# Performance work log

Measured on AMD Instinct MI355X. Metric: run time of the kernel, lower is better.

## Reference

```python
import jax, jax.numpy as jnp
import numpy as np

D_MODEL = 192
NODE_NUM = 64
DEPTH = 2
ALPHA = 0.05
NUM_LAYERS = 2
LN_EPS = 1e-5


def _gcn(x, p):
    # x: [N, in_dim*D_MODEL]; faithful port of GCN.forward (eval mode)
    nv1, nv2, ws, bs, wm, bm, we, be, wl, bl, g, b = p
    N = x.shape[0]
    in_dim = x.shape[1] // D_MODEL
    adp = jax.nn.softmax(jax.nn.relu(nv1 @ nv2), axis=1)            # [V,V]
    adj = adp + jnp.eye(NODE_NUM, dtype=x.dtype)
    a = adj / adj.sum(1, keepdims=True)                              # row-normalized
    h0 = jax.lax.conv_general_dilated(
        x.reshape(N, in_dim, D_MODEL), ws, (1,), 'VALID',
        dimension_numbers=('NCH', 'OIH', 'NCH')) + bs[None, :, None]  # [N,C,V]
    h = h0
    outs = [h0]
    for _ in range(DEPTH):
        h = ALPHA * h0 + (1.0 - ALPHA) * jnp.einsum('ncw,vw->ncv', h, a)
        outs.append(h)
    ho = jnp.concatenate(outs, axis=1)                               # [N,(DEPTH+1)C,V]
    ho = jax.nn.gelu(jnp.einsum('ncv,oc->nov', ho, wm) + bm[None, :, None], approximate=False)
    ho = jnp.einsum('ncv,oc->nov', ho, we) + be[None, :, None]       # [N,6,V]
    ho = jnp.einsum('nov,dv->nod', ho, wl) + bl                      # [N,6,D]
    mu = ho.mean(-1, keepdims=True)
    var = ((ho - mu) ** 2).mean(-1, keepdims=True)                   # biased, like torch LN
    ho = (ho - mu) / jnp.sqrt(var + LN_EPS) * g + b
    return ho.reshape(N, 6 * D_MODEL)


def _encoder(inp4, flag, layer_params):
    x = jnp.transpose(inp4, (2, 0, 1, 3)) if flag == 1 else jnp.transpose(inp4, (1, 0, 2, 3))
    W, B, O, D = x.shape
    L = W + O - 1
    N = W * B
    # input_transfer: shift row r by r along the slice axis
    place = jax.vmap(lambda xr, r: jax.lax.dynamic_update_slice(
        jnp.zeros((B, L, D), x.dtype), xr, (0, r, 0)))
    a = place(x, jnp.arange(W)).reshape(N, L, D)
    layer0_output = None
    output_all = None
    rows_layers, cols_layers = [], []
    for layer in range(NUM_LAYERS):
        if layer >= 1:
            a = output_all  # eval mode: F.dropout is identity
            if layer == 1:
                layer0_output = a
        p = layer_params[layer]

        def step(carry, x_t, p=p):
            h_row, h_col = carry
            gate = _gcn(jnp.concatenate([h_row, h_col, x_t], axis=-1), p)  # [N,6D]
            sg = jax.nn.sigmoid(gate[:, :4 * D])
            tg = jnp.tanh(gate[:, 4 * D:])
            ug_r, og_r, ug_c, og_c = jnp.split(sg, 4, axis=-1)
            ig_r, ig_c = jnp.split(tg, 2, axis=-1)
            h_row = jnp.tanh((1.0 - ug_r) * h_row + ug_r * ig_r) * og_r
            h_col = jnp.tanh((1.0 - ug_c) * h_col + ug_c * ig_c) * og_c
            out_s = jnp.concatenate([h_row, h_col], axis=-1)
            # col hidden is saved pre-roll, rolled for next step
            return (h_row, jnp.roll(h_col, B, axis=0)), (out_s, h_row, h_col)

        init = (jnp.zeros((N, D), x.dtype), jnp.zeros((N, D), x.dtype))
        _, (outs, hrows, hcols) = jax.lax.scan(step, init, jnp.swapaxes(a, 0, 1))
        output_all = jnp.swapaxes(outs, 0, 1)                        # [N,L,2D]
        if layer >= 1:
            output_all = output_all + layer0_output
        # rows saved at slice s>=O-1 from block loc = s-O+1
        rows = hrows.reshape(L, W, B, D)[jnp.arange(O - 1, L), jnp.arange(W)]  # [W,B,D]
        # cols saved at slice s>=W-1 from last batch block
        cols = hcols[W - 1:, (W - 1) * B:, :]                        # [O,B,D]
        rows_layers.append(rows)
        cols_layers.append(cols)
    hidden_row_all = jnp.stack(rows_layers).transpose(2, 0, 1, 3)    # [B,layers,W,D]
    hidden_col_all = jnp.stack(cols_layers).transpose(2, 0, 1, 3)    # [B,layers,O,D]
    if flag == 1:
        return output_all, hidden_col_all, hidden_row_all
    return output_all, hidden_row_all, hidden_col_all


def setup_inputs() -> dict:
    key = jax.random.key(0)
    ks = jax.random.split(key, 20)
    idx = [0]
    def nxt():
        k = ks[idx[0]]
        idx[0] += 1
        return k
    B, W, O = 8, 24, 48
    K = D_MODEL - NODE_NUM + 1  # 129
    cc, sc, nd = 16, 32, 40
    d = {"input": jax.random.normal(nxt(), (B, W, O, D_MODEL), dtype=jnp.float32)}
    for li, in_dim in enumerate([3, 4]):
        d[f"nodevec1_{li}"] = jax.random.normal(nxt(), (NODE_NUM, nd), dtype=jnp.float32)
        d[f"nodevec2_{li}"] = jax.random.normal(nxt(), (nd, NODE_NUM), dtype=jnp.float32)
        d[f"w_start_{li}"] = jax.random.normal(nxt(), (cc, in_dim, K), dtype=jnp.float32) * 0.05
        d[f"b_start_{li}"] = jnp.zeros((cc,), jnp.float32)
        d[f"w_mlp_{li}"] = jax.random.normal(nxt(), (sc, (DEPTH + 1) * cc), dtype=jnp.float32) * 0.05
        d[f"b_mlp_{li}"] = jnp.zeros((sc,), jnp.float32)
        d[f"w_end_{li}"] = jax.random.normal(nxt(), (6, sc), dtype=jnp.float32) * 0.05
        d[f"b_end_{li}"] = jnp.zeros((6,), jnp.float32)
        d[f"w_lin_{li}"] = jax.random.normal(nxt(), (D_MODEL, NODE_NUM), dtype=jnp.float32) * 0.05
        d[f"b_lin_{li}"] = jnp.zeros((D_MODEL,), jnp.float32)
        d[f"gamma_{li}"] = jnp.ones((D_MODEL,), jnp.float32)
        d[f"beta_{li}"] = jnp.zeros((D_MODEL,), jnp.float32)
    d["flag"] = 0
    return d


def reference(input, nodevec1_0, nodevec2_0, w_start_0, b_start_0, w_mlp_0, b_mlp_0,
              w_end_0, b_end_0, w_lin_0, b_lin_0, gamma_0, beta_0,
              nodevec1_1, nodevec2_1, w_start_1, b_start_1, w_mlp_1, b_mlp_1,
              w_end_1, b_end_1, w_lin_1, b_lin_1, gamma_1, beta_1, flag):
    p0 = (nodevec1_0, nodevec2_0, w_start_0, b_start_0, w_mlp_0, b_mlp_0,
          w_end_0, b_end_0, w_lin_0, b_lin_0, gamma_0, beta_0)
    p1 = (nodevec1_1, nodevec2_1, w_start_1, b_start_1, w_mlp_1, b_mlp_1,
          w_end_1, b_end_1, w_lin_1, b_lin_1, gamma_1, beta_1)
    return _encoder(input, flag, (p0, p1))
```

## Files before the change

### kernel.cpp

```cpp
#include <hip/hip_runtime.h>
#include <hip/hip_bf16.h>

#define NT 512
typedef unsigned short u16;
typedef unsigned long long u64;

__device__ __forceinline__ u16 tobf(float x) {
  union { __hip_bfloat16 h; u16 u; } cv;
  cv.h = __float2bfloat16(x);
  return cv.u;
}
__device__ __forceinline__ float frombf(u16 u) {
  return __uint_as_float(((unsigned)u) << 16);
}
__device__ __forceinline__ float sigf(float x) {
  return __builtin_amdgcn_rcpf(1.f + __builtin_amdgcn_exp2f(-1.4426950408889634f * x));
}
__device__ __forceinline__ float tanh_fast(float x) {
  return 1.f - 2.f * __builtin_amdgcn_rcpf(1.f + __builtin_amdgcn_exp2f(2.8853900817779268f * x));
}
__device__ __forceinline__ void lds_fence() {
  asm volatile("s_waitcnt lgkmcnt(0)" ::: "memory");
  __builtin_amdgcn_sched_barrier(0);
}
__device__ __forceinline__ void bar_light() {
  asm volatile("s_waitcnt lgkmcnt(0)" ::: "memory");
  __builtin_amdgcn_s_barrier();
  asm volatile("" ::: "memory");
}

__device__ __forceinline__ void conv4(const float* __restrict__ wrow,
                                      const float* __restrict__ xin,
                                      float& a0, float& a1, float& a2, float& a3) {
  float4 xc = *(const float4*)xin;
  for (int k4 = 0; k4 < 128; k4 += 4) {
    float4 wv = *(const float4*)(wrow + k4);
    float4 xn = *(const float4*)(xin + k4 + 4);
    a0 = fmaf(wv.w, xc.w, fmaf(wv.z, xc.z, fmaf(wv.y, xc.y, fmaf(wv.x, xc.x, a0))));
    a1 = fmaf(wv.w, xn.x, fmaf(wv.z, xc.w, fmaf(wv.y, xc.z, fmaf(wv.x, xc.y, a1))));
    a2 = fmaf(wv.w, xn.y, fmaf(wv.z, xn.x, fmaf(wv.y, xc.w, fmaf(wv.x, xc.z, a2))));
    a3 = fmaf(wv.w, xn.z, fmaf(wv.z, xn.y, fmaf(wv.y, xn.x, fmaf(wv.x, xc.w, a3))));
    xc = xn;
  }
  float wk = wrow[128];
  a0 = fmaf(wk, xc.x, a0); a1 = fmaf(wk, xc.y, a1);
  a2 = fmaf(wk, xc.z, a2); a3 = fmaf(wk, xc.w, a3);
}

struct SeqArgs {
  const float* input;
  const float* nv1_0; const float* nv2_0; const float* nv1_1; const float* nv2_1;
  const float* w_start0; const float* b_start0; const float* w_mlp0; const float* b_mlp0;
  const float* w_end0;   const float* b_end0;   const float* w_lin0; const float* b_lin0;
  const float* gamma0;   const float* beta0;
  const float* w_start1; const float* b_start1; const float* w_mlp1; const float* b_mlp1;
  const float* w_end1;   const float* b_end1;   const float* w_lin1; const float* b_lin1;
  const float* gamma1;   const float* beta1;
  u64*   HCOL2;
  int*   prog;
  float* out_all; float* out_hrow; float* out_hcol;
};

__global__ __launch_bounds__(NT, 2) void seq_kernel(SeqArgs A) {
  const int n = blockIdx.x, w = n >> 3, b = n & 7, tid = threadIdx.x;
  const int pred = (n + 184) % 192;
  const int succ = (n + 8) % 192;

  __shared__ __align__(16) float sCIN[384];
  __shared__ __align__(16) float sXB[2][384];
  __shared__ __align__(16) float sWSf[64 * 132];
  __shared__ __align__(16) float sAT[4096];
  __shared__ __align__(16) float sH[2][1024];
  __shared__ __align__(16) float sPreP[2048];
  __shared__ __align__(16) float sAbuf[4928];
  float* const sPart = sAbuf;
  float* const sG    = sAbuf;
  float* const sH2c  = sAbuf + 2048;
  float* const sE    = sAbuf + 2048;
  float* const sY    = sAbuf;
  float* const smWE  = sAbuf + 3072;
  float* const smBE  = sAbuf + 3264;
  float* const smWM  = sAbuf + 3328;

  for (int layer = 0; layer < 2; ++layer) {
    const int in_dim = 3 + layer;
    const int P = in_dim - 1;
    const float* nv1    = layer ? A.nv1_1    : A.nv1_0;
    const float* nv2    = layer ? A.nv2_1    : A.nv2_0;
    const float* wstart = layer ? A.w_start1 : A.w_start0;
    const float* bs     = layer ? A.b_start1 : A.b_start0;
    const float* wm     = layer ? A.w_mlp1   : A.w_mlp0;
    const float* bm     = layer ? A.b_mlp1   : A.b_mlp0;
    const float* we     = layer ? A.w_end1   : A.w_end0;
    const float* be     = layer ? A.b_end1   : A.b_end0;
    const float* wl     = layer ? A.w_lin1   : A.w_lin0;
    const float* bl     = layer ? A.b_lin1   : A.b_lin0;
    const float* gm     = layer ? A.gamma1   : A.gamma0;
    const float* bt     = layer ? A.beta1    : A.beta0;

    for (int idx = tid; idx < 4096; idx += NT) {
      int v = idx >> 6, ww = idx & 63;
      float s = 0.f;
      for (int j = 0; j < 40; ++j) s = fmaf(nv1[v*40 + j], nv2[j*64 + ww], s);
      sAbuf[idx] = fmaxf(s, 0.f);
    }
    __syncthreads();
    if (tid < 64) {
      const int v = tid;
      float m = -1e30f;
      for (int ww = 0; ww < 64; ++ww) m = fmaxf(m, sAbuf[v*64 + ww]);
      float s = 0.f;
      for (int ww = 0; ww < 64; ++ww) { float e = expf(sAbuf[v*64 + ww] - m); sAbuf[v*64 + ww] = e; s += e; }
      float inv = 1.f / s, rs = 1.f;
      for (int ww = 0; ww < 64; ++ww) rs += sAbuf[v*64 + ww] * inv;
      float irs = 1.f / rs;
      for (int ww = 0; ww < 64; ++ww) {
        float a = sAbuf[v*64 + ww] * inv + ((ww == v) ? 1.f : 0.f);
        sAT[ww*64 + v] = a * irs;
      }
    }
    __syncthreads();
    for (int idx = tid; idx < 16*in_dim*132; idx += NT) {
      int row = idx / 132, k = idx - row*132;
      sWSf[idx] = (k < 129) ? frombf(tobf(wstart[((row & 15)*in_dim + (row >> 4))*129 + k])) : 0.f;
    }
    for (int idx = tid; idx < 1536; idx += NT) { int o = idx/48, c = idx - o*48; smWM[o*50 + c] = wm[idx]; }
    for (int idx = tid; idx < 192; idx += NT) smWE[idx] = we[idx];
    if (tid < 6) smBE[tid] = be[tid];
    for (int d = tid; d < 384; d += NT) sCIN[d] = 0.f;

    const int v_p = tid & 63;
    const int o0  = tid >> 6;
    const float bmv0 = bm[o0], bmv1 = bm[o0 + 8], bmv2 = bm[o0 + 16], bmv3 = bm[o0 + 24];
    float blv = 0.f, gmv = 1.f, btv = 0.f;
    if (tid < 384) blv = bl[(tid >= 192) ? tid - 192 : tid];
    if (tid < 192) { gmv = gm[tid]; btv = bt[tid]; }
    float bs_r[2];
    bs_r[0] = bs[tid >> 6];
    bs_r[1] = bs[(tid >> 6) + 8];
    __syncthreads();

    {
      if (layer == 0) {
        int o = 0 - w;
        for (int d = tid; d < 192; d += NT)
          sXB[0][d] = (o >= 0 && o < 48) ? A.input[(((size_t)(b*24 + w)*48 + o)*192) + d] : 0.f;
      } else {
        for (int d = tid; d < 384; d += NT)
          sXB[0][d] = A.out_all[((size_t)n*71 + 0)*384 + d];
      }
      bar_light();
      const int nslots = P << 8;
      for (int s = tid; s < nslots; s += NT) {
        const int cidx = s >> 4;
        const int p = cidx >> 4, c = cidx & 15;
        const int vg = s & 15;
        const int ich = (p == 0) ? 0 : (p + 1);
        const float* xin = ((p == 0) ? &sCIN[0] : &sXB[0][(p-1)*192]) + vg*4;
        float a0 = 0.f, a1 = 0.f, a2 = 0.f, a3 = 0.f;
        conv4(&sWSf[(ich*16 + c)*132], xin, a0, a1, a2, a3);
        float* dst = (p == 0) ? &sPart[c*64 + vg*4] : &sPreP[(p-1)*1024 + c*64 + vg*4];
        *(float4*)dst = make_float4(a0, a1, a2, a3);
      }
      bar_light();
      {
        const int c0 = tid >> 6, v = tid & 63;
        float sum0 = bs_r[0], sum1 = bs_r[1];
        sum0 += sPart[c0*64 + v];
        sum1 += sPart[(c0+8)*64 + v];
        for (int p = 1; p < P; ++p) {
          sum0 += sPreP[(p-1)*1024 + c0*64 + v];
          sum1 += sPreP[(p-1)*1024 + (c0+8)*64 + v];
        }
        sH[0][ c0     *64 + v] = sum0;
        sH[0][(c0 + 8)*64 + v] = sum1;
      }
      bar_light();
    }

    for (int t = 0; t < 71; ++t) {
      const int S = layer*71 + t;

      float xpa = 0.f, xpb = 0.f;
      if (t < 70 && tid >= 256 && tid < 448) {
        const int d = tid - 256;
        if (layer == 0) {
          int o = (t + 1) - w;
          if (o >= 0 && o < 48)
            xpa = A.input[(((size_t)(b*24 + w)*48 + o)*192) + d];
        } else {
          const float* xr = A.out_all + ((size_t)n*71 + (t+1))*384;
          xpa = xr[d];
          xpb = xr[192 + d];
        }
      }
      if (t > 0) {
        if (tid < 192) {
          const u64* src = &A.HCOL2[((size_t)((S-1) & 15)*192 + pred)*192 + tid];
          u64 v = __hip_atomic_load(src, __ATOMIC_RELAXED, __HIP_MEMORY_SCOPE_AGENT);
          while ((unsigned)(v >> 32) != (unsigned)S) {
            __builtin_amdgcn_s_sleep(1);
            v = __hip_atomic_load(src, __ATOMIC_RELAXED, __HIP_MEMORY_SCOPE_AGENT);
          }
          __builtin_amdgcn_sched_barrier(0);
          asm volatile("" ::: "memory");
          sCIN[192 + tid] = __uint_as_float((unsigned)v);
        } else if (tid == 448 && S >= 16) {
          while (__hip_atomic_load(&A.prog[succ*32], __ATOMIC_RELAXED, __HIP_MEMORY_SCOPE_AGENT) < S - 15)
            __builtin_amdgcn_s_sleep(2);
        }
        bar_light();
        if (tid == 0)
          __hip_atomic_store(&A.prog[n*32], S, __ATOMIC_RELAXED, __HIP_MEMORY_SCOPE_AGENT);
      } else if (S >= 16) {
        if (tid == 448) {
          while (__hip_atomic_load(&A.prog[succ*32], __ATOMIC_RELAXED, __HIP_MEMORY_SCOPE_AGENT) < S - 15)
            __builtin_amdgcn_s_sleep(2);
        }
      }

      {
        const int c = tid >> 5, vg2 = tid & 31;
        const int vbase = c*64 + vg2*2;
        const float* xin = &sCIN[192 + vg2*2];
        const float* wrow = &sWSf[(16 + c)*132];
        float a0 = sH[0][vbase], a1 = sH[0][vbase + 1];
        float2 xc = *(const float2*)xin;
        for (int k2 = 0; k2 < 128; k2 += 2) {
          float2 wv = *(const float2*)(wrow + k2);
          float2 xn = *(const float2*)(xin + k2 + 2);
          a0 = fmaf(wv.y, xc.y, fmaf(wv.x, xc.x, a0));
          a1 = fmaf(wv.y, xn.x, fmaf(wv.x, xc.y, a1));
          xc = xn;
        }
        float wk = wrow[128];
        a0 = fmaf(wk, xc.x, a0); a1 = fmaf(wk, xc.y, a1);
        sH[0][vbase] = a0; sH[0][vbase + 1] = a1;
      }
      lds_fence();
      {
        const int c0 = o0 * 2;
        float pa0 = 0.f, pa1 = 0.f;
        for (int w4 = 0; w4 < 64; w4 += 4) {
          float a0v = sAT[(w4+0)*64 + v_p];
          float a1v = sAT[(w4+1)*64 + v_p];
          float a2v = sAT[(w4+2)*64 + v_p];
          float a3v = sAT[(w4+3)*64 + v_p];
          float4 h0v = *(const float4*)&sH[0][ c0      *64 + w4];
          float4 h1v = *(const float4*)&sH[0][(c0 + 1 )*64 + w4];
          pa0 = fmaf(h0v.x, a0v, pa0); pa0 = fmaf(h0v.y, a1v, pa0);
          pa0 = fmaf(h0v.z, a2v, pa0); pa0 = fmaf(h0v.w, a3v, pa0);
          pa1 = fmaf(h1v.x, a0v, pa1); pa1 = fmaf(h1v.y, a1v, pa1);
          pa1 = fmaf(h1v.z, a2v, pa1); pa1 = fmaf(h1v.w, a3v, pa1);
        }
        float h0a = sH[0][ c0      *64 + v_p];
        float h0b = sH[0][(c0 + 1 )*64 + v_p];
        sH[1][ c0      *64 + v_p] = fmaf(0.95f, pa0, 0.05f * h0a);
        sH[1][(c0 + 1 )*64 + v_p] = fmaf(0.95f, pa1, 0.05f * h0b);
        lds_fence();
        float pb0 = 0.f, pb1 = 0.f;
        for (int w4 = 0; w4 < 64; w4 += 4) {
          float a0v = sAT[(w4+0)*64 + v_p];
          float a1v = sAT[(w4+1)*64 + v_p];
          float a2v = sAT[(w4+2)*64 + v_p];
          float a3v = sAT[(w4+3)*64 + v_p];
          float4 h0v = *(const float4*)&sH[1][ c0      *64 + w4];
          float4 h1v = *(const float4*)&sH[1][(c0 + 1 )*64 + w4];
          pb0 = fmaf(h0v.x, a0v, pb0); pb0 = fmaf(h0v.y, a1v, pb0);
          pb0 = fmaf(h0v.z, a2v, pb0); pb0 = fmaf(h0v.w, a3v, pb0);
          pb1 = fmaf(h1v.x, a0v, pb1); pb1 = fmaf(h1v.y, a1v, pb1);
          pb1 = fmaf(h1v.z, a2v, pb1); pb1 = fmaf(h1v.w, a3v, pb1);
        }
        sH2c[ c0      *64 + v_p] = fmaf(0.95f, pb0, 0.05f * h0a);
        sH2c[(c0 + 1 )*64 + v_p] = fmaf(0.95f, pb1, 0.05f * h0b);
      }
      bar_light();

      {
        float g0 = bmv0, g1 = bmv1, g2 = bmv2, g3 = bmv3;
#pragma unroll
        for (int c = 0; c < 16; ++c) {
          float h0v = sH[0][c*64 + v_p];
          float h1v = sH[1][c*64 + v_p];
          float h2v = sH2c[c*64 + v_p];
          g0 = fmaf(smWM[(o0     )*50 + c], h0v, fmaf(smWM[(o0     )*50 + 16 + c], h1v, fmaf(smWM[(o0     )*50 + 32 + c], h2v, g0)));
          g1 = fmaf(smWM[(o0 +  8)*50 + c], h0v, fmaf(smWM[(o0 +  8)*50 + 16 + c], h1v, fmaf(smWM[(o0 +  8)*50 + 32 + c], h2v, g1)));
          g2 = fmaf(smWM[(o0 + 16)*50 + c], h0v, fmaf(smWM[(o0 + 16)*50 + 16 + c], h1v, fmaf(smWM[(o0 + 16)*50 + 32 + c], h2v, g2)));
          g3 = fmaf(smWM[(o0 + 24)*50 + c], h0v, fmaf(smWM[(o0 + 24)*50 + 16 + c], h1v, fmaf(smWM[(o0 + 24)*50 + 32 + c], h2v, g3)));
        }
        g0 = 0.5f * g0 * (1.f + erff(g0 * 0.70710678118654752f));
        g1 = 0.5f * g1 * (1.f + erff(g1 * 0.70710678118654752f));
        g2 = 0.5f * g2 * (1.f + erff(g2 * 0.70710678118654752f));
        g3 = 0.5f * g3 * (1.f + erff(g3 * 0.70710678118654752f));
        sG[(o0     )*64 + v_p] = g0;
        sG[(o0 +  8)*64 + v_p] = g1;
        sG[(o0 + 16)*64 + v_p] = g2;
        sG[(o0 + 24)*64 + v_p] = g3;
      }
      bar_light();

      for (int idx = tid; idx < 384; idx += NT) {
        int o2 = idx >> 6, v = idx & 63;
        float acc = smBE[o2];
        for (int c = 0; c < 32; ++c) acc = fmaf(smWE[o2*32 + c], sG[c*64 + v], acc);
        sE[idx] = acc;
      }
      bar_light();

      if (tid < 384) {
        const int d  = (tid >= 192) ? tid - 192 : tid;
        const int r0 = (tid >= 192) ? 3 : 0;
        const float4* wrow = (const float4*)(wl + d*64);
        float y0 = blv, y1 = blv, y2 = blv;
        for (int q = 0; q < 16; ++q) {
          float4 wv = wrow[q];
          float4 e0 = *(const float4*)&sE[(r0+0)*64 + q*4];
          float4 e1 = *(const float4*)&sE[(r0+1)*64 + q*4];
          float4 e2 = *(const float4*)&sE[(r0+2)*64 + q*4];
          y0 = fmaf(e0.x,wv.x, fmaf(e0.y,wv.y, fmaf(e0.z,wv.z, fmaf(e0.w,wv.w, y0))));
          y1 = fmaf(e1.x,wv.x, fmaf(e1.y,wv.y, fmaf(e1.z,wv.z, fmaf(e1.w,wv.w, y1))));
          y2 = fmaf(e2.x,wv.x, fmaf(e2.y,wv.y, fmaf(e2.z,wv.z, fmaf(e2.w,wv.w, y2))));
        }
        sY[(r0+0)*192 + d] = y0;
        sY[(r0+1)*192 + d] = y1;
        sY[(r0+2)*192 + d] = y2;
      }
      bar_light();

      if (tid < 192) {
        const int r = tid >> 5, l32 = tid & 31;
        float sm = 0.f, sq = 0.f;
#pragma unroll
        for (int m = 0; m < 6; ++m) {
          float v = sY[r*192 + l32 + 32*m];
          sm += v; sq = fmaf(v, v, sq);
        }
#pragma unroll
        for (int off = 16; off >= 1; off >>= 1) {
          sm += __shfl_xor(sm, off);
          sq += __shfl_xor(sq, off);
        }
        if (l32 == 0) {
          float mu = sm * (1.f/192.f);
          float var = sq * (1.f/192.f) - mu*mu;
          sH[1][r] = mu;
          sH[1][8 + r] = rsqrtf(fmaxf(var, 0.f) + 1e-5f);
        }
      }
      bar_light();

      float hcn = 0.f;
      if (tid < 192) {
        const int d = tid;
        float y2 = fmaf((sY[2*192+d] - sH[1][2]) * sH[1][10], gmv, btv);
        float y3 = fmaf((sY[3*192+d] - sH[1][3]) * sH[1][11], gmv, btv);
        float y5 = fmaf((sY[5*192+d] - sH[1][5]) * sH[1][13], gmv, btv);
        float ugc = sigf(y2), ogc = sigf(y3), igc = tanh_fast(y5);
        float hc = sCIN[192 + d];
        hcn = tanh_fast(fmaf(ugc, igc, (1.f - ugc)*hc)) * ogc;
        u64 pk = ((u64)(unsigned)(S + 1) << 32) | (u64)__float_as_uint(hcn);
        __hip_atomic_store(&A.HCOL2[((size_t)(S & 15)*192 + n)*192 + d], pk,
                           __ATOMIC_RELAXED, __HIP_MEMORY_SCOPE_AGENT);
      } else if (t < 70 && tid >= 256 && tid < 448) {
        const int d = tid - 256;
        float* xbn = &sXB[(t+1) & 1][0];
        xbn[d] = xpa;
        if (layer == 1) xbn[192 + d] = xpb;
      }
      bar_light();

      if (tid < 192) {
        const int d = tid;
        float y0 = fmaf((sY[0*192+d] - sH[1][0]) * sH[1][8],  gmv, btv);
        float y1 = fmaf((sY[1*192+d] - sH[1][1]) * sH[1][9],  gmv, btv);
        float y4 = fmaf((sY[4*192+d] - sH[1][4]) * sH[1][12], gmv, btv);
        float ugr = sigf(y0), ogr = sigf(y1), igr = tanh_fast(y4);
        float hr = sCIN[d];
        float hrn = tanh_fast(fmaf(ugr, igr, (1.f - ugr)*hr)) * ogr;
        sCIN[d] = hrn;
        float* oa = A.out_all + ((size_t)n*71 + t)*384;
        if (layer == 0) { oa[d] = hrn; oa[192 + d] = hcn; }
        else {
          const float* xbt = &sXB[t & 1][0];
          oa[d] = hrn + xbt[d]; oa[192 + d] = hcn + xbt[192 + d];
        }
        if (t == 47 + w)
          A.out_hrow[(((size_t)b*2 + layer)*24 + w)*192 + d] = hrn;
        if (w == 23 && t >= 23)
          A.out_hcol[(((size_t)b*2 + layer)*48 + (t - 23))*192 + d] = hcn;
      } else if (t < 70 && tid >= 192 && tid < 448) {
        const int sl = tid - 192;
        const int nx = (P - 1) << 8;
        const float* xbn = &sXB[(t+1) & 1][0];
        for (int s = sl; s < nx; s += 256) {
          const int p = 1 + (s >> 8);
          const int c = (s >> 4) & 15, vg = s & 15;
          const int ich = p + 1;
          float a0 = 0.f, a1 = 0.f, a2 = 0.f, a3 = 0.f;
          conv4(&sWSf[(ich*16 + c)*132], &xbn[(p-1)*192 + vg*4], a0, a1, a2, a3);
          *(float4*)&sPreP[(p-1)*1024 + c*64 + vg*4] = make_float4(a0, a1, a2, a3);
        }
      }
      bar_light();

      if (t < 70) {
        if (tid < 256) {
          const int c = tid >> 4, vg = tid & 15;
          float a0 = 0.f, a1 = 0.f, a2 = 0.f, a3 = 0.f;
          conv4(&sWSf[c*132], &sCIN[vg*4], a0, a1, a2, a3);
          *(float4*)&sPart[c*64 + vg*4] = make_float4(a0, a1, a2, a3);
        }
        bar_light();
        {
          const int c0 = tid >> 6, v = tid & 63;
          float sum0 = bs_r[0], sum1 = bs_r[1];
          sum0 += sPart[c0*64 + v];
          sum1 += sPart[(c0+8)*64 + v];
          for (int p = 1; p < P; ++p) {
            sum0 += sPreP[(p-1)*1024 + c0*64 + v];
            sum1 += sPreP[(p-1)*1024 + (c0+8)*64 + v];
          }
          sH[0][ c0     *64 + v] = sum0;
          sH[0][(c0 + 8)*64 + v] = sum1;
        }
        bar_light();
      }
    }
    __syncthreads();
  }
}

extern "C" void kernel_launch(void* const* d_in, const int* in_sizes, int n_in,
                              void* d_out, int out_size, void* d_ws, size_t ws_size,
                              hipStream_t stream) {
  (void)in_sizes; (void)n_in; (void)out_size; (void)ws_size;
  char* ws = (char*)d_ws;
  int* prog  = (int*)ws;
  u64* HCOL2 = (u64*)(ws + 24576);

  (void)hipMemsetAsync(ws, 0, 24576 + 4718592, stream);

  SeqArgs A;
  A.input    = (const float*)d_in[0];
  A.nv1_0    = (const float*)d_in[1];  A.nv2_0 = (const float*)d_in[2];
  A.w_start0 = (const float*)d_in[3];  A.b_start0 = (const float*)d_in[4];
  A.w_mlp0   = (const float*)d_in[5];  A.b_mlp0   = (const float*)d_in[6];
  A.w_end0   = (const float*)d_in[7];  A.b_end0   = (const float*)d_in[8];
  A.w_lin0   = (const float*)d_in[9];  A.b_lin0   = (const float*)d_in[10];
  A.gamma0   = (const float*)d_in[11]; A.beta0    = (const float*)d_in[12];
  A.nv1_1    = (const float*)d_in[13]; A.nv2_1 = (const float*)d_in[14];
  A.w_start1 = (const float*)d_in[15]; A.b_start1 = (const float*)d_in[16];
  A.w_mlp1   = (const float*)d_in[17]; A.b_mlp1   = (const float*)d_in[18];
  A.w_end1   = (const float*)d_in[19]; A.b_end1   = (const float*)d_in[20];
  A.w_lin1   = (const float*)d_in[21]; A.b_lin1   = (const float*)d_in[22];
  A.gamma1   = (const float*)d_in[23]; A.beta1    = (const float*)d_in[24];
  A.HCOL2 = HCOL2; A.prog = prog;
  A.out_all  = (float*)d_out;
  A.out_hrow = (float*)d_out + 5234688;
  A.out_hcol = (float*)d_out + 5308416;

  seq_kernel<<<192, NT, 0, stream>>>(A);
}
```

Measured before the change: 2.672 ms.

## Restructure per-step schedule to cut barriers and overlap cross-block wait

```diff
diff --git a/kernel.cpp b/kernel.cpp
--- a/kernel.cpp
+++ b/kernel.cpp
@@ -67,7 +67,6 @@
   const int succ = (n + 8) % 192;
 
   __shared__ __align__(16) float sCIN[384];
-  __shared__ __align__(16) float sXB[2][384];
   __shared__ __align__(16) float sWSf[64 * 132];
   __shared__ __align__(16) float sAT[4096];
   __shared__ __align__(16) float sH[2][1024];
@@ -78,6 +77,7 @@
   float* const sH2c  = sAbuf + 2048;
   float* const sE    = sAbuf + 2048;
   float* const sY    = sAbuf;
+  float* const sLN   = sAbuf + 2432;
   float* const smWE  = sAbuf + 3072;
   float* const smBE  = sAbuf + 3264;
   float* const smWM  = sAbuf + 3328;
@@ -132,99 +132,55 @@
     const int v_p = tid & 63;
     const int o0  = tid >> 6;
     const float bmv0 = bm[o0], bmv1 = bm[o0 + 8], bmv2 = bm[o0 + 16], bmv3 = bm[o0 + 24];
+    const float bs_c = bs[tid >> 5];
     float blv = 0.f, gmv = 1.f, btv = 0.f;
     if (tid < 384) blv = bl[(tid >= 192) ? tid - 192 : tid];
     if (tid < 192) { gmv = gm[tid]; btv = bt[tid]; }
-    float bs_r[2];
-    bs_r[0] = bs[tid >> 6];
-    bs_r[1] = bs[(tid >> 6) + 8];
     __syncthreads();
 
-    {
-      if (layer == 0) {
-        int o = 0 - w;
-        for (int d = tid; d < 192; d += NT)
-          sXB[0][d] = (o >= 0 && o < 48) ? A.input[(((size_t)(b*24 + w)*48 + o)*192) + d] : 0.f;
-      } else {
-        for (int d = tid; d < 384; d += NT)
-          sXB[0][d] = A.out_all[((size_t)n*71 + 0)*384 + d];
-      }
-      bar_light();
-      const int nslots = P << 8;
-      for (int s = tid; s < nslots; s += NT) {
-        const int cidx = s >> 4;
-        const int p = cidx >> 4, c = cidx & 15;
-        const int vg = s & 15;
-        const int ich = (p == 0) ? 0 : (p + 1);
-        const float* xin = ((p == 0) ? &sCIN[0] : &sXB[0][(p-1)*192]) + vg*4;
+    if (tid >= 256) {
+      const int i = tid - 256;
+      *(float4*)&sPart[i*4] = make_float4(0.f, 0.f, 0.f, 0.f);
+    } else if (tid >= 192) {
+    }
+    if (tid >= 192 && tid < 448) {
+      const int sl = tid - 192;
+      const int nx = (P - 1) << 8;
+      for (int s = sl; s < nx; s += 256) {
+        const int p = 1 + (s >> 8), c = (s >> 4) & 15, vg = s & 15;
         float a0 = 0.f, a1 = 0.f, a2 = 0.f, a3 = 0.f;
-        conv4(&sWSf[(ich*16 + c)*132], xin, a0, a1, a2, a3);
-        float* dst = (p == 0) ? &sPart[c*64 + vg*4] : &sPreP[(p-1)*1024 + c*64 + vg*4];
-        *(float4*)dst = make_float4(a0, a1, a2, a3);
-      }
-      bar_light();
-      {
-        const int c0 = tid >> 6, v = tid & 63;
-        float sum0 = bs_r[0], sum1 = bs_r[1];
-        sum0 += sPart[c0*64 + v];
-        sum1 += sPart[(c0+8)*64 + v];
-        for (int p = 1; p < P; ++p) {
-          sum0 += sPreP[(p-1)*1024 + c0*64 + v];
-          sum1 += sPreP[(p-1)*1024 + (c0+8)*64 + v];
-        }
-        sH[0][ c0     *64 + v] = sum0;
-        sH[0][(c0 + 8)*64 + v] = sum1;
-      }
-      bar_light();
-    }
+        if (layer == 0) {
+          int o = 0 - w;
+          if (o >= 0 && o < 48)
+            conv4(&sWSf[((p+1)*16 + c)*132],
+                  A.input + (((size_t)(b*24 + w)*48 + o)*192) + vg*4, a0, a1, a2, a3);
+        } else {
+          conv4(&sWSf[((p+1)*16 + c)*132],
+                A.out_all + ((size_t)n*71 + 0)*384 + (p-1)*192 + vg*4, a0, a1, a2, a3);
+        }
+        *(float4*)&sPreP[(p-1)*1024 + c*64 + vg*4] = make_float4(a0, a1, a2, a3);
+      }
+    }
+    if (tid == 0 && layer == 1) {
+      while (__hip_atomic_load(&A.prog[succ*32], __ATOMIC_RELAXED, __HIP_MEMORY_SCOPE_AGENT) < 56)
+        __builtin_amdgcn_s_sleep(2);
+    }
+    bar_light();
 
     for (int t = 0; t < 71; ++t) {
       const int S = layer*71 + t;
-
-      float xpa = 0.f, xpb = 0.f;
-      if (t < 70 && tid >= 256 && tid < 448) {
-        const int d = tid - 256;
-        if (layer == 0) {
-          int o = (t + 1) - w;
-          if (o >= 0 && o < 48)
-            xpa = A.input[(((size_t)(b*24 + w)*48 + o)*192) + d];
-        } else {
-          const float* xr = A.out_all + ((size_t)n*71 + (t+1))*384;
-          xpa = xr[d];
-          xpb = xr[192 + d];
-        }
-      }
-      if (t > 0) {
-        if (tid < 192) {
-          const u64* src = &A.HCOL2[((size_t)((S-1) & 15)*192 + pred)*192 + tid];
-          u64 v = __hip_atomic_load(src, __ATOMIC_RELAXED, __HIP_MEMORY_SCOPE_AGENT);
-          while ((unsigned)(v >> 32) != (unsigned)S) {
-            __builtin_amdgcn_s_sleep(1);
-            v = __hip_atomic_load(src, __ATOMIC_RELAXED, __HIP_MEMORY_SCOPE_AGENT);
-          }
-          __builtin_amdgcn_sched_barrier(0);
-          asm volatile("" ::: "memory");
-          sCIN[192 + tid] = __uint_as_float((unsigned)v);
-        } else if (tid == 448 && S >= 16) {
-          while (__hip_atomic_load(&A.prog[succ*32], __ATOMIC_RELAXED, __HIP_MEMORY_SCOPE_AGENT) < S - 15)
-            __builtin_amdgcn_s_sleep(2);
-        }
-        bar_light();
-        if (tid == 0)
-          __hip_atomic_store(&A.prog[n*32], S, __ATOMIC_RELAXED, __HIP_MEMORY_SCOPE_AGENT);
-      } else if (S >= 16) {
-        if (tid == 448) {
-          while (__hip_atomic_load(&A.prog[succ*32], __ATOMIC_RELAXED, __HIP_MEMORY_SCOPE_AGENT) < S - 15)
-            __builtin_amdgcn_s_sleep(2);
-        }
-      }
 
       {
         const int c = tid >> 5, vg2 = tid & 31;
         const int vbase = c*64 + vg2*2;
+        float a0 = bs_c + sPart[vbase];
+        float a1 = bs_c + sPart[vbase + 1];
+        for (int p = 1; p < P; ++p) {
+          a0 += sPreP[(p-1)*1024 + vbase];
+          a1 += sPreP[(p-1)*1024 + vbase + 1];
+        }
         const float* xin = &sCIN[192 + vg2*2];
         const float* wrow = &sWSf[(16 + c)*132];
-        float a0 = sH[0][vbase], a1 = sH[0][vbase + 1];
         float2 xc = *(const float2*)xin;
         for (int k2 = 0; k2 < 128; k2 += 2) {
           float2 wv = *(const float2*)(wrow + k2);
@@ -299,17 +255,18 @@
       }
       bar_light();
 
-      for (int idx = tid; idx < 384; idx += NT) {
-        int o2 = idx >> 6, v = idx & 63;
+      if (tid < 384) {
+        int o2 = tid >> 6, v = tid & 63;
         float acc = smBE[o2];
         for (int c = 0; c < 32; ++c) acc = fmaf(smWE[o2*32 + c], sG[c*64 + v], acc);
-        sE[idx] = acc;
+        sE[tid] = acc;
       }
       bar_light();
 
       if (tid < 384) {
         const int d  = (tid >= 192) ? tid - 192 : tid;
         const int r0 = (tid >= 192) ? 3 : 0;
+        const int part = (tid >= 192) ? ((tid - 192) >> 6) : (tid >> 6);
         const float4* wrow = (const float4*)(wl + d*64);
         float y0 = blv, y1 = blv, y2 = blv;
         for (int q = 0; q < 16; ++q) {
@@ -324,106 +281,102 @@
         sY[(r0+0)*192 + d] = y0;
         sY[(r0+1)*192 + d] = y1;
         sY[(r0+2)*192 + d] = y2;
+        float ys0 = y0, ys1 = y1, ys2 = y2;
+        float q0 = y0*y0, q1 = y1*y1, q2 = y2*y2;
+#pragma unroll
+        for (int off = 32; off >= 1; off >>= 1) {
+          ys0 += __shfl_xor(ys0, off); q0 += __shfl_xor(q0, off);
+          ys1 += __shfl_xor(ys1, off); q1 += __shfl_xor(q1, off);
+          ys2 += __shfl_xor(ys2, off); q2 += __shfl_xor(q2, off);
+        }
+        if ((tid & 63) == 0) {
+          sLN[(r0+0)*6 + part] = ys0; sLN[(r0+0)*6 + 3 + part] = q0;
+          sLN[(r0+1)*6 + part] = ys1; sLN[(r0+1)*6 + 3 + part] = q1;
+          sLN[(r0+2)*6 + part] = ys2; sLN[(r0+2)*6 + 3 + part] = q2;
+        }
       }
       bar_light();
 
       if (tid < 192) {
-        const int r = tid >> 5, l32 = tid & 31;
-        float sm = 0.f, sq = 0.f;
+        const int d = tid;
+        float* oa = A.out_all + ((size_t)n*71 + t)*384;
+        float r0v = 0.f, r1v = 0.f;
+        if (layer == 1) { r0v = oa[d]; r1v = oa[192 + d]; }
+        float muA[6], sgA[6];
 #pragma unroll
-        for (int m = 0; m < 6; ++m) {
-          float v = sY[r*192 + l32 + 32*m];
-          sm += v; sq = fmaf(v, v, sq);
-        }
-#pragma unroll
-        for (int off = 16; off >= 1; off >>= 1) {
-          sm += __shfl_xor(sm, off);
-          sq += __shfl_xor(sq, off);
-        }
-        if (l32 == 0) {
+        for (int r = 0; r < 6; ++r) {
+          float sm = (sLN[r*6 + 0] + sLN[r*6 + 1]) + sLN[r*6 + 2];
+          float sq = (sLN[r*6 + 3] + sLN[r*6 + 4]) + sLN[r*6 + 5];
           float mu = sm * (1.f/192.f);
           float var = sq * (1.f/192.f) - mu*mu;
-          sH[1][r] = mu;
-          sH[1][8 + r] = rsqrtf(fmaxf(var, 0.f) + 1e-5f);
-        }
-      }
-      bar_light();
-
-      float hcn = 0.f;
-      if (tid < 192) {
-        const int d = tid;
-        float y2 = fmaf((sY[2*192+d] - sH[1][2]) * sH[1][10], gmv, btv);
-        float y3 = fmaf((sY[3*192+d] - sH[1][3]) * sH[1][11], gmv, btv);
-        float y5 = fmaf((sY[5*192+d] - sH[1][5]) * sH[1][13], gmv, btv);
+          muA[r] = mu;
+          sgA[r] = rsqrtf(fmaxf(var, 0.f) + 1e-5f);
+        }
+        float y2 = fmaf((sY[2*192+d] - muA[2]) * sgA[2], gmv, btv);
+        float y3 = fmaf((sY[3*192+d] - muA[3]) * sgA[3], gmv, btv);
+        float y5 = fmaf((sY[5*192+d] - muA[5]) * sgA[5], gmv, btv);
         float ugc = sigf(y2), ogc = sigf(y3), igc = tanh_fast(y5);
         float hc = sCIN[192 + d];
-        hcn = tanh_fast(fmaf(ugc, igc, (1.f - ugc)*hc)) * ogc;
+        float hcn = tanh_fast(fmaf(ugc, igc, (1.f - ugc)*hc)) * ogc;
         u64 pk = ((u64)(unsigned)(S + 1) << 32) | (u64)__float_as_uint(hcn);
         __hip_atomic_store(&A.HCOL2[((size_t)(S & 15)*192 + n)*192 + d], pk,
                            __ATOMIC_RELAXED, __HIP_MEMORY_SCOPE_AGENT);
-      } else if (t < 70 && tid >= 256 && tid < 448) {
-        const int d = tid - 256;
-        float* xbn = &sXB[(t+1) & 1][0];
-        xbn[d] = xpa;
-        if (layer == 1) xbn[192 + d] = xpb;
-      }
-      bar_light();
-
-      if (tid < 192) {
-        const int d = tid;
-        float y0 = fmaf((sY[0*192+d] - sH[1][0]) * sH[1][8],  gmv, btv);
-        float y1 = fmaf((sY[1*192+d] - sH[1][1]) * sH[1][9],  gmv, btv);
-        float y4 = fmaf((sY[4*192+d] - sH[1][4]) * sH[1][12], gmv, btv);
+        float y0 = fmaf((sY[0*192+d] - muA[0]) * sgA[0], gmv, btv);
+        float y1 = fmaf((sY[1*192+d] - muA[1]) * sgA[1], gmv, btv);
+        float y4 = fmaf((sY[4*192+d] - muA[4]) * sgA[4], gmv, btv);
         float ugr = sigf(y0), ogr = sigf(y1), igr = tanh_fast(y4);
         float hr = sCIN[d];
         float hrn = tanh_fast(fmaf(ugr, igr, (1.f - ugr)*hr)) * ogr;
         sCIN[d] = hrn;
-        float* oa = A.out_all + ((size_t)n*71 + t)*384;
         if (layer == 0) { oa[d] = hrn; oa[192 + d] = hcn; }
-        else {
-          const float* xbt = &sXB[t & 1][0];
-          oa[d] = hrn + xbt[d]; oa[192 + d] = hcn + xbt[192 + d];
-        }
+        else           { oa[d] = hrn + r0v; oa[192 + d] = hcn + r1v; }
         if (t == 47 + w)
           A.out_hrow[(((size_t)b*2 + layer)*24 + w)*192 + d] = hrn;
         if (w == 23 && t >= 23)
           A.out_hcol[(((size_t)b*2 + layer)*48 + (t - 23))*192 + d] = hcn;
-      } else if (t < 70 && tid >= 192 && tid < 448) {
+      } else if (tid < 448 && t < 70) {
         const int sl = tid - 192;
         const int nx = (P - 1) << 8;
-        const float* xbn = &sXB[(t+1) & 1][0];
         for (int s = sl; s < nx; s += 256) {
-          const int p = 1 + (s >> 8);
-          const int c = (s >> 4) & 15, vg = s & 15;
-          const int ich = p + 1;
+          const int p = 1 + (s >> 8), c = (s >> 4) & 15, vg = s & 15;
           float a0 = 0.f, a1 = 0.f, a2 = 0.f, a3 = 0.f;
-          conv4(&sWSf[(ich*16 + c)*132], &xbn[(p-1)*192 + vg*4], a0, a1, a2, a3);
+          if (layer == 0) {
+            int o = (t + 1) - w;
+            if (o >= 0 && o < 48)
+              conv4(&sWSf[((p+1)*16 + c)*132],
+                    A.input + (((size_t)(b*24 + w)*48 + o)*192) + vg*4, a0, a1, a2, a3);
+          } else {
+            conv4(&sWSf[((p+1)*16 + c)*132],
+                  A.out_all + ((size_t)n*71 + (t+1))*384 + (p-1)*192 + vg*4, a0, a1, a2, a3);
+          }
           *(float4*)&sPreP[(p-1)*1024 + c*64 + vg*4] = make_float4(a0, a1, a2, a3);
         }
       }
       bar_light();
 
       if (t < 70) {
-        if (tid < 256) {
-          const int c = tid >> 4, vg = tid & 15;
+        if (tid < 192) {
+          const u64* src = &A.HCOL2[((size_t)(S & 15)*192 + pred)*192 + tid];
+          u64 v = __hip_atomic_load(src, __ATOMIC_RELAXED, __HIP_MEMORY_SCOPE_AGENT);
+          while ((unsigned)(v >> 32) != (unsigned)(S + 1)) {
+            __builtin_amdgcn_s_sleep(1);
+            v = __hip_atomic_load(src, __ATOMIC_RELAXED, __HIP_MEMORY_SCOPE_AGENT);
+          }
+          __builtin_amdgcn_sched_barrier(0);
+          asm volatile("" ::: "memory");
+          sCIN[192 + tid] = __uint_as_float((unsigned)v);
+        } else if (tid >= 256) {
+          const int c = (tid >> 4) & 15, vg = tid & 15;
           float a0 = 0.f, a1 = 0.f, a2 = 0.f, a3 = 0.f;
           conv4(&sWSf[c*132], &sCIN[vg*4], a0, a1, a2, a3);
           *(float4*)&sPart[c*64 + vg*4] = make_float4(a0, a1, a2, a3);
+        } else if (tid == 200 && S + 1 >= 16) {
+          while (__hip_atomic_load(&A.prog[succ*32], __ATOMIC_RELAXED, __HIP_MEMORY_SCOPE_AGENT) < S - 14)
+            __builtin_amdgcn_s_sleep(2);
         }
         bar_light();
-        {
-          const int c0 = tid >> 6, v = tid & 63;
-          float sum0 = bs_r[0], sum1 = bs_r[1];
-          sum0 += sPart[c0*64 + v];
-          sum1 += sPart[(c0+8)*64 + v];
-          for (int p = 1; p < P; ++p) {
-            sum0 += sPreP[(p-1)*1024 + c0*64 + v];
-            sum1 += sPreP[(p-1)*1024 + (c0+8)*64 + v];
-          }
-          sH[0][ c0     *64 + v] = sum0;
-          sH[0][(c0 + 8)*64 + v] = sum1;
-        }
-        bar_light();
+        if (tid == 0)
+          __hip_atomic_store(&A.prog[n*32], S + 1, __ATOMIC_RELAXED, __HIP_MEMORY_SCOPE_AGENT);
       }
     }
     __syncthreads();
```

Measured after the change: 2.923 ms. +9.4%, slower.
